# Optimization experiments

Hardware: AMD Instinct MI355X
Metric: run time of the kernel (lower is better)

Reference implementation:

```python
import jax, jax.numpy as jnp
import numpy as np

LEN = 8388608  # 2**23, must be a power of 2


def setup_inputs() -> dict:
    key = jax.random.key(0)
    k1, k2 = jax.random.split(key)
    inp = jax.random.normal(k1, (LEN,), dtype=jnp.float32)
    weight = jax.random.uniform(k2, (LEN // 2, 2), dtype=jnp.float32)  # learned twiddle factors
    return {"input": inp, "weight": weight}


def _complex_mul(a, w):
    # a: [d, cols, 2] complex pairs; w: [cols, 2] broadcast over leading dim
    ar, ai = a[:, :, 0], a[:, :, 1]
    wr, wi = w[:, 0], w[:, 1]
    return jnp.stack([ar * wr - ai * wi, ar * wi + ai * wr], axis=-1)


def reference(input, weight):
    n = input.shape[0]
    # real signal -> complex pairs, shape [n, 1, 2]
    x = jnp.stack([input, jnp.zeros_like(input)], axis=-1)[:, None, :]
    d = n // 2
    while d != 0:  # log2(n) static stages
        w = weight[0::d]          # [cols, 2] where cols == x.shape[1]
        top = x[:d]               # [d, cols, 2]
        bot = x[d:]               # [d, cols, 2]
        p = _complex_mul(bot, w)  # butterfly twiddle multiply
        x = jnp.concatenate([top + p, top - p], axis=1)  # [d, 2*cols, 2]
        d //= 2
    return x  # [1, n, 2]
```

## Files before the change

### kernel.cpp

```cpp
#include <hip/hip_runtime.h>
#include <hip/hip_fp16.h>

__device__ __forceinline__ float2 cadd(float2 a, float2 b) { return make_float2(a.x + b.x, a.y + b.y); }
__device__ __forceinline__ float2 csub(float2 a, float2 b) { return make_float2(a.x - b.x, a.y - b.y); }
__device__ __forceinline__ float2 cmul(float2 w, float2 z) {
    return make_float2(w.x * z.x - w.y * z.y, w.x * z.y + w.y * z.x);
}
__device__ __forceinline__ unsigned pk(float2 z) {
    __half2 h = __floats2half2_rn(z.x, z.y);
    return *reinterpret_cast<unsigned*>(&h);
}
__device__ __forceinline__ float2 upk(unsigned u) {
    __half2 h = *reinterpret_cast<__half2*>(&u);
    return __half22float2(h);
}


__global__ __launch_bounds__(256) void fft_pass_a(const float* __restrict__ in,
                                                  const float2* __restrict__ wt,
                                                  uint4* __restrict__ outp)
{
    __shared__ float2 L[4096];
    const int tid = threadIdx.x;
    const int l0  = blockIdx.x << 4;
    const int c   = tid & 15;
    const int qb  = tid >> 4;

    float2 pw1[4], pw2a[4], pw2b[4];
#pragma unroll
    for (int k = 0; k < 4; ++k) { pw1[k] = wt[0]; pw2a[k] = wt[0]; pw2b[k] = wt[1 << 21]; }

    {
        const int c4 = tid & 3, gg = tid >> 2;
#pragma unroll
        for (int k = 0; k < 4; ++k) {
            const int g = gg + (k << 6);
            const float4 v = *reinterpret_cast<const float4*>(in + ((size_t)g << 15) + l0 + (c4 << 2));
            const int base = (g << 4) + (c4 << 2);
            L[base + 0] = make_float2(v.x, 0.f);
            L[base + 1] = make_float2(v.y, 0.f);
            L[base + 2] = make_float2(v.z, 0.f);
            L[base + 3] = make_float2(v.w, 0.f);
        }
    }
    __syncthreads();

#pragma unroll
    for (int rho = 0; rho < 4; ++rho) {
        const int s = rho << 1, H = 128 >> s, Q = H >> 1, lo = 6 - s;
        float2 nw1[4], nw2a[4], nw2b[4];
        if (rho < 3) {
            const int s2 = s + 2, lo2 = 6 - s2;
#pragma unroll
            for (int k = 0; k < 4; ++k) {
                const int qi = (qb << 2) + k;
                const int b  = ((qi >> lo2) << (lo2 + 2)) | (qi & ((1 << lo2) - 1));
                const int jl = (int)(__brev((unsigned)(b >> (8 - s2))) >> (32 - s2));
                const int e  = jl << (21 - s2);
                nw1[k] = wt[e << 1]; nw2a[k] = wt[e]; nw2b[k] = wt[e + (1 << 21)];
            }
        }
#pragma unroll
        for (int k = 0; k < 4; ++k) {
            const int qi = (qb << 2) + k;
            const int b  = ((qi >> lo) << (lo + 2)) | (qi & ((1 << lo) - 1));
            const int iA = (b << 4) + c;
            const float2 A  = L[iA];
            const float2 Bv = L[iA + (Q << 4)];
            const float2 Cv = L[iA + (H << 4)];
            const float2 Dv = L[iA + ((H + Q) << 4)];
            const float2 pC = cmul(pw1[k], Cv), pD = cmul(pw1[k], Dv);
            const float2 tA = cadd(A, pC),  tC = csub(A, pC);
            const float2 tB = cadd(Bv, pD), tD = csub(Bv, pD);
            const float2 p2 = cmul(pw2a[k], tB);
            const float2 p3 = cmul(pw2b[k], tD);
            L[iA]                  = cadd(tA, p2);
            L[iA + (Q << 4)]       = csub(tA, p2);
            L[iA + (H << 4)]       = cadd(tC, p3);
            L[iA + ((H + Q) << 4)] = csub(tC, p3);
        }
        __syncthreads();
        if (rho < 3) {
#pragma unroll
            for (int k = 0; k < 4; ++k) { pw1[k] = nw1[k]; pw2a[k] = nw2a[k]; pw2b[k] = nw2b[k]; }
        }
    }

    {
        const int c4 = tid & 3, gg = tid >> 2;
#pragma unroll
        for (int k = 0; k < 4; ++k) {
            const int g  = gg + (k << 6);
            const int li = (g << 4) + (c4 << 2);
            uint4 v;
            v.x = pk(L[li]); v.y = pk(L[li + 1]); v.z = pk(L[li + 2]); v.w = pk(L[li + 3]);
            outp[((size_t)g << 13) + (l0 >> 2) + c4] = v;
        }
    }
}

__global__ __launch_bounds__(256) void fft_pass_b(const uint4* __restrict__ inp,
                                                  const float2* __restrict__ wt,
                                                  uint4* __restrict__ outp)
{
    __shared__ float2 L[4096];
    const int tid  = threadIdx.x;
    const int h    = blockIdx.x >> 3;
    const int l0   = (blockIdx.x & 7) << 4;
    const int hrev = (int)(__brev((unsigned)h) >> 24);
    const int c  = tid & 15;
    const int qb = tid >> 4;
    const size_t pbase = ((size_t)h << 13) + (l0 >> 2);

    float2 pw1[4], pw2a[4], pw2b[4];
    {
        const int e0 = hrev << 13;
#pragma unroll
        for (int k = 0; k < 4; ++k) { pw1[k] = wt[e0 << 1]; pw2a[k] = wt[e0]; pw2b[k] = wt[e0 + (1 << 21)]; }
    }

    {
        const int c4 = tid & 3, gg = tid >> 2;
#pragma unroll
        for (int k = 0; k < 4; ++k) {
            const int g = gg + (k << 6);
            const uint4 v = inp[pbase + (g << 5) + c4];
            const int li = (g << 4) + (c4 << 2);
            L[li]     = upk(v.x);
            L[li + 1] = upk(v.y);
            L[li + 2] = upk(v.z);
            L[li + 3] = upk(v.w);
        }
    }
    __syncthreads();

#pragma unroll
    for (int rho = 0; rho < 4; ++rho) {
        const int s = rho << 1, H = 128 >> s, Q = H >> 1, lo = 6 - s;
        float2 nw1[4], nw2a[4], nw2b[4];
        if (rho < 3) {
            const int s2 = s + 2, lo2 = 6 - s2;
#pragma unroll
            for (int k = 0; k < 4; ++k) {
                const int qi = (qb << 2) + k;
                const int b  = ((qi >> lo2) << (lo2 + 2)) | (qi & ((1 << lo2) - 1));
                const int jl = (int)(__brev((unsigned)(b >> (8 - s2))) >> (32 - s2));
                const int e  = (hrev << (13 - s2)) + (jl << (21 - s2));
                nw1[k] = wt[e << 1]; nw2a[k] = wt[e]; nw2b[k] = wt[e + (1 << 21)];
            }
        }
#pragma unroll
        for (int k = 0; k < 4; ++k) {
            const int qi = (qb << 2) + k;
            const int b  = ((qi >> lo) << (lo + 2)) | (qi & ((1 << lo) - 1));
            const int iA = (b << 4) + c;
            const float2 A  = L[iA];
            const float2 Bv = L[iA + (Q << 4)];
            const float2 Cv = L[iA + (H << 4)];
            const float2 Dv = L[iA + ((H + Q) << 4)];
            const float2 pC = cmul(pw1[k], Cv), pD = cmul(pw1[k], Dv);
            const float2 tA = cadd(A, pC),  tC = csub(A, pC);
            const float2 tB = cadd(Bv, pD), tD = csub(Bv, pD);
            const float2 p2 = cmul(pw2a[k], tB);
            const float2 p3 = cmul(pw2b[k], tD);
            L[iA]                  = cadd(tA, p2);
            L[iA + (Q << 4)]       = csub(tA, p2);
            L[iA + (H << 4)]       = cadd(tC, p3);
            L[iA + ((H + Q) << 4)] = csub(tC, p3);
        }
        __syncthreads();
        if (rho < 3) {
#pragma unroll
            for (int k = 0; k < 4; ++k) { pw1[k] = nw1[k]; pw2a[k] = nw2a[k]; pw2b[k] = nw2b[k]; }
        }
    }

    {
        const int c4 = tid & 3, gg = tid >> 2;
#pragma unroll
        for (int k = 0; k < 4; ++k) {
            const int g  = gg + (k << 6);
            const int li = (g << 4) + (c4 << 2);
            uint4 v;
            v.x = pk(L[li]); v.y = pk(L[li + 1]); v.z = pk(L[li + 2]); v.w = pk(L[li + 3]);
            outp[pbase + (g << 5) + c4] = v;
        }
    }
}

__global__ __launch_bounds__(256, 8) void fft_pass_c(const uint4* __restrict__ inp,
                                                     const float2* __restrict__ wt,
                                                     float2* __restrict__ out)
{
    __shared__ float2 L[16 * 129];
    const int tid = threadIdx.x;
    const int h0  = blockIdx.x;

    const int lam = tid & 15;
    const int bq  = tid >> 4;
    const int rH  = (h0 << 4) + lam;

    float2 pw1[2], pw2a[2], pw2b[2];
#pragma unroll
    for (int k = 0; k < 2; ++k) {
        pw1[k]  = wt[rH << 6];
        pw2a[k] = wt[rH << 5];
        pw2b[k] = wt[(rH << 5) + (1 << 21)];
    }

    {
        const int f  = tid & 31;
        const int ll = tid >> 5;
#pragma unroll
        for (int k = 0; k < 2; ++k) {
            const int lm = ll + (k << 3);
            const int H  = (int)(__brev((unsigned)((h0 << 4) + lm)) >> 16);
            const uint4 v = inp[((size_t)H << 5) + f];
            const int li = lm * 129 + (f << 2);
            L[li]     = upk(v.x);
            L[li + 1] = upk(v.y);
            L[li + 2] = upk(v.z);
            L[li + 3] = upk(v.w);
        }
    }
    __syncthreads();

    float2 pr2[4];
#pragma unroll
    for (int rho = 0; rho < 3; ++rho) {
        const int s = rho << 1, H = 64 >> s, Q = H >> 1, lo = 5 - s;
        float2 nw1[2], nw2a[2], nw2b[2];
        if (rho < 2) {
            const int s2 = s + 2, lo2 = 5 - s2;
#pragma unroll
            for (int k = 0; k < 2; ++k) {
                const int qi = (bq << 1) + k;
                const int b  = ((qi >> lo2) << (lo2 + 2)) | (qi & ((1 << lo2) - 1));
                const int jl = (int)(__brev((unsigned)(b >> (7 - s2))) >> (32 - s2));
                const int e  = (rH << (5 - s2)) + (jl << (21 - s2));
                nw1[k] = wt[e << 1]; nw2a[k] = wt[e]; nw2b[k] = wt[e + (1 << 21)];
            }
        } else {
#pragma unroll
            for (int k = 0; k < 4; ++k) {
                const int pb = (bq << 2) + k;
                const int jl = (int)(__brev((unsigned)pb) >> 26);
                pr2[k] = wt[rH + (jl << 16)];
            }
        }
#pragma unroll
        for (int k = 0; k < 2; ++k) {
            const int qi = (bq << 1) + k;
            const int b  = ((qi >> lo) << (lo + 2)) | (qi & ((1 << lo) - 1));
            const int iA = lam * 129 + b;
            const float2 A  = L[iA];
            const float2 Bv = L[iA + Q];
            const float2 Cv = L[iA + H];
            const float2 Dv = L[iA + H + Q];
            const float2 pC = cmul(pw1[k], Cv), pD = cmul(pw1[k], Dv);
            const float2 tA = cadd(A, pC),  tC = csub(A, pC);
            const float2 tB = cadd(Bv, pD), tD = csub(Bv, pD);
            const float2 p2 = cmul(pw2a[k], tB);
            const float2 p3 = cmul(pw2b[k], tD);
            L[iA]         = cadd(tA, p2);
            L[iA + Q]     = csub(tA, p2);
            L[iA + H]     = cadd(tC, p3);
            L[iA + H + Q] = csub(tC, p3);
        }
        __syncthreads();
        if (rho < 2) {
#pragma unroll
            for (int k = 0; k < 2; ++k) { pw1[k] = nw1[k]; pw2a[k] = nw2a[k]; pw2b[k] = nw2b[k]; }
        }
    }

    {
#pragma unroll
        for (int k = 0; k < 4; ++k) {
            const int pb = (bq << 2) + k;
            const int b  = pb << 1;
            const int iA = lam * 129 + b;
            const float2 A  = L[iA];
            const float2 Bv = L[iA + 1];
            const float2 p  = cmul(pr2[k], Bv);
            L[iA]     = cadd(A, p);
            L[iA + 1] = csub(A, p);
        }
    }
    __syncthreads();

    {
        const int l2 = (tid & 7) << 1;
        const int gb = tid >> 3;
#pragma unroll
        for (int k = 0; k < 4; ++k) {
            const int g    = gb + (k << 5);
            const int grev = (int)(__brev((unsigned)g) >> 25);
            const float2 a0 = L[l2 * 129 + g];
            const float2 a1 = L[(l2 + 1) * 129 + g];
            const size_t o = ((size_t)grev << 16) + (h0 << 4) + l2;
            *reinterpret_cast<float4*>(out + o) = make_float4(a0.x, a0.y, a1.x, a1.y);
        }
    }
}

extern "C" void kernel_launch(void* const* d_in, const int* in_sizes, int n_in,
                              void* d_out, int out_size, void* d_ws, size_t ws_size,
                              hipStream_t stream)
{
    (void)in_sizes; (void)n_in; (void)out_size; (void)ws_size;
    const float*  in = (const float*)d_in[0];
    const float2* wt = (const float2*)d_in[1];
    float2* outc = (float2*)d_out;
    uint4*  buf1 = (uint4*)d_ws;
    uint4*  buf2 = (uint4*)((char*)d_ws + (32u << 20));

    fft_pass_a<<<2048, 256, 0, stream>>>(in,   wt, buf1);
    fft_pass_b<<<2048, 256, 0, stream>>>(buf1, wt, buf2);
    fft_pass_c<<<4096, 256, 0, stream>>>(buf2, wt, outc);
}
```

Measured before the change: 182.4 us.

## Fuse FFT passes B and C into one register-resident 15-stage kernel

Replaces the second and third FFT passes with a single kernel in which each 1024-thread block processes a 32K-point sub-FFT. The work is split into three 5-stage radix-2 groups held in registers, separated by skewed shared-memory transposes. This removes one global-memory round trip through the fp16 intermediate buffer and one kernel launch. The cost is heavy register use (96 complex values per thread), only 256 blocks, 128KB of dynamic shared memory per block, and uncoalesced-looking strided final output writes.

```diff
diff --git a/kernel.cpp b/kernel.cpp
--- a/kernel.cpp
+++ b/kernel.cpp
@@ -13,6 +13,12 @@
 __device__ __forceinline__ float2 upk(unsigned u) {
     __half2 h = *reinterpret_cast<__half2*>(&u);
     return __half22float2(h);
+}
+
+__host__ __device__ constexpr unsigned crev(unsigned x, int bits) {
+    unsigned r = 0;
+    for (int k = 0; k < bits; ++k) r |= ((x >> k) & 1u) << (bits - 1 - k);
+    return r;
 }
 
 
@@ -99,208 +105,122 @@
     }
 }
 
-__global__ __launch_bounds__(256) void fft_pass_b(const uint4* __restrict__ inp,
-                                                  const float2* __restrict__ wt,
-                                                  uint4* __restrict__ outp)
+__global__ __launch_bounds__(1024) void fft_pass_bc(const unsigned* __restrict__ inp,
+                                                    const float2* __restrict__ wt,
+                                                    float2* __restrict__ out)
 {
-    __shared__ float2 L[4096];
-    const int tid  = threadIdx.x;
-    const int h    = blockIdx.x >> 3;
-    const int l0   = (blockIdx.x & 7) << 4;
-    const int hrev = (int)(__brev((unsigned)h) >> 24);
-    const int c  = tid & 15;
-    const int qb = tid >> 4;
-    const size_t pbase = ((size_t)h << 13) + (l0 >> 2);
-
-    float2 pw1[4], pw2a[4], pw2b[4];
-    {
-        const int e0 = hrev << 13;
-#pragma unroll
-        for (int k = 0; k < 4; ++k) { pw1[k] = wt[e0 << 1]; pw2a[k] = wt[e0]; pw2b[k] = wt[e0 + (1 << 21)]; }
-    }
-
-    {
-        const int c4 = tid & 3, gg = tid >> 2;
-#pragma unroll
-        for (int k = 0; k < 4; ++k) {
-            const int g = gg + (k << 6);
-            const uint4 v = inp[pbase + (g << 5) + c4];
-            const int li = (g << 4) + (c4 << 2);
-            L[li]     = upk(v.x);
-            L[li + 1] = upk(v.y);
-            L[li + 2] = upk(v.z);
-            L[li + 3] = upk(v.w);
-        }
-    }
-    __syncthreads();
-
-#pragma unroll
-    for (int rho = 0; rho < 4; ++rho) {
-        const int s = rho << 1, H = 128 >> s, Q = H >> 1, lo = 6 - s;
-        float2 nw1[4], nw2a[4], nw2b[4];
-        if (rho < 3) {
-            const int s2 = s + 2, lo2 = 6 - s2;
-#pragma unroll
-            for (int k = 0; k < 4; ++k) {
-                const int qi = (qb << 2) + k;
-                const int b  = ((qi >> lo2) << (lo2 + 2)) | (qi & ((1 << lo2) - 1));
-                const int jl = (int)(__brev((unsigned)(b >> (8 - s2))) >> (32 - s2));
-                const int e  = (hrev << (13 - s2)) + (jl << (21 - s2));
-                nw1[k] = wt[e << 1]; nw2a[k] = wt[e]; nw2b[k] = wt[e + (1 << 21)];
-            }
-        }
-#pragma unroll
-        for (int k = 0; k < 4; ++k) {
-            const int qi = (qb << 2) + k;
-            const int b  = ((qi >> lo) << (lo + 2)) | (qi & ((1 << lo) - 1));
-            const int iA = (b << 4) + c;
-            const float2 A  = L[iA];
-            const float2 Bv = L[iA + (Q << 4)];
-            const float2 Cv = L[iA + (H << 4)];
-            const float2 Dv = L[iA + ((H + Q) << 4)];
-            const float2 pC = cmul(pw1[k], Cv), pD = cmul(pw1[k], Dv);
-            const float2 tA = cadd(A, pC),  tC = csub(A, pC);
-            const float2 tB = cadd(Bv, pD), tD = csub(Bv, pD);
-            const float2 p2 = cmul(pw2a[k], tB);
-            const float2 p3 = cmul(pw2b[k], tD);
-            L[iA]                  = cadd(tA, p2);
-            L[iA + (Q << 4)]       = csub(tA, p2);
-            L[iA + (H << 4)]       = cadd(tC, p3);
-            L[iA + ((H + Q) << 4)] = csub(tC, p3);
-        }
-        __syncthreads();
-        if (rho < 3) {
-#pragma unroll
-            for (int k = 0; k < 4; ++k) { pw1[k] = nw1[k]; pw2a[k] = nw2a[k]; pw2b[k] = nw2b[k]; }
-        }
-    }
-
-    {
-        const int c4 = tid & 3, gg = tid >> 2;
-#pragma unroll
-        for (int k = 0; k < 4; ++k) {
-            const int g  = gg + (k << 6);
-            const int li = (g << 4) + (c4 << 2);
-            uint4 v;
-            v.x = pk(L[li]); v.y = pk(L[li + 1]); v.z = pk(L[li + 2]); v.w = pk(L[li + 3]);
-            outp[pbase + (g << 5) + c4] = v;
-        }
-    }
-}
-
-__global__ __launch_bounds__(256, 8) void fft_pass_c(const uint4* __restrict__ inp,
-                                                     const float2* __restrict__ wt,
-                                                     float2* __restrict__ out)
-{
-    __shared__ float2 L[16 * 129];
+    extern __shared__ float2 T[];
     const int tid = threadIdx.x;
-    const int h0  = blockIdx.x;
-
-    const int lam = tid & 15;
-    const int bq  = tid >> 4;
-    const int rH  = (h0 << 4) + lam;
-
-    float2 pw1[2], pw2a[2], pw2b[2];
-#pragma unroll
-    for (int k = 0; k < 2; ++k) {
-        pw1[k]  = wt[rH << 6];
-        pw2a[k] = wt[rH << 5];
-        pw2b[k] = wt[(rH << 5) + (1 << 21)];
-    }
-
-    {
-        const int f  = tid & 31;
-        const int ll = tid >> 5;
-#pragma unroll
-        for (int k = 0; k < 2; ++k) {
-            const int lm = ll + (k << 3);
-            const int H  = (int)(__brev((unsigned)((h0 << 4) + lm)) >> 16);
-            const uint4 v = inp[((size_t)H << 5) + f];
-            const int li = lm * 129 + (f << 2);
-            L[li]     = upk(v.x);
-            L[li + 1] = upk(v.y);
-            L[li + 2] = upk(v.z);
-            L[li + 3] = upk(v.w);
-        }
-    }
-    __syncthreads();
-
-    float2 pr2[4];
-#pragma unroll
-    for (int rho = 0; rho < 3; ++rho) {
-        const int s = rho << 1, H = 64 >> s, Q = H >> 1, lo = 5 - s;
-        float2 nw1[2], nw2a[2], nw2b[2];
-        if (rho < 2) {
-            const int s2 = s + 2, lo2 = 5 - s2;
-#pragma unroll
-            for (int k = 0; k < 2; ++k) {
-                const int qi = (bq << 1) + k;
-                const int b  = ((qi >> lo2) << (lo2 + 2)) | (qi & ((1 << lo2) - 1));
-                const int jl = (int)(__brev((unsigned)(b >> (7 - s2))) >> (32 - s2));
-                const int e  = (rH << (5 - s2)) + (jl << (21 - s2));
-                nw1[k] = wt[e << 1]; nw2a[k] = wt[e]; nw2b[k] = wt[e + (1 << 21)];
-            }
-        } else {
-#pragma unroll
-            for (int k = 0; k < 4; ++k) {
-                const int pb = (bq << 2) + k;
-                const int jl = (int)(__brev((unsigned)pb) >> 26);
-                pr2[k] = wt[rH + (jl << 16)];
-            }
-        }
-#pragma unroll
-        for (int k = 0; k < 2; ++k) {
-            const int qi = (bq << 1) + k;
-            const int b  = ((qi >> lo) << (lo + 2)) | (qi & ((1 << lo) - 1));
-            const int iA = lam * 129 + b;
-            const float2 A  = L[iA];
-            const float2 Bv = L[iA + Q];
-            const float2 Cv = L[iA + H];
-            const float2 Dv = L[iA + H + Q];
-            const float2 pC = cmul(pw1[k], Cv), pD = cmul(pw1[k], Dv);
-            const float2 tA = cadd(A, pC),  tC = csub(A, pC);
-            const float2 tB = cadd(Bv, pD), tD = csub(Bv, pD);
-            const float2 p2 = cmul(pw2a[k], tB);
-            const float2 p3 = cmul(pw2b[k], tD);
-            L[iA]         = cadd(tA, p2);
-            L[iA + Q]     = csub(tA, p2);
-            L[iA + H]     = cadd(tC, p3);
-            L[iA + H + Q] = csub(tC, p3);
-        }
-        __syncthreads();
-        if (rho < 2) {
-#pragma unroll
-            for (int k = 0; k < 2; ++k) { pw1[k] = nw1[k]; pw2a[k] = nw2a[k]; pw2b[k] = nw2b[k]; }
-        }
-    }
-
-    {
-#pragma unroll
-        for (int k = 0; k < 4; ++k) {
-            const int pb = (bq << 2) + k;
-            const int b  = pb << 1;
-            const int iA = lam * 129 + b;
-            const float2 A  = L[iA];
-            const float2 Bv = L[iA + 1];
-            const float2 p  = cmul(pr2[k], Bv);
-            L[iA]     = cadd(A, p);
-            L[iA + 1] = csub(A, p);
-        }
-    }
-    __syncthreads();
-
-    {
-        const int l2 = (tid & 7) << 1;
-        const int gb = tid >> 3;
-#pragma unroll
-        for (int k = 0; k < 4; ++k) {
-            const int g    = gb + (k << 5);
-            const int grev = (int)(__brev((unsigned)g) >> 25);
-            const float2 a0 = L[l2 * 129 + g];
-            const float2 a1 = L[(l2 + 1) * 129 + g];
-            const size_t o = ((size_t)grev << 16) + (h0 << 4) + l2;
-            *reinterpret_cast<float4*>(out + o) = make_float4(a0.x, a0.y, a1.x, a1.y);
-        }
+    const int h   = blockIdx.x;
+    const unsigned hrev = __brev((unsigned)h) >> 24;
+
+    float2 X[32];
+    {
+        const unsigned base = ((unsigned)h << 15) + (unsigned)tid;
+#pragma unroll
+        for (int b = 0; b < 32; ++b) X[b] = upk(inp[base + ((unsigned)b << 10)]);
+    }
+
+#pragma unroll
+    for (int s1 = 0; s1 < 5; ++s1) {
+        const int beta = 4 - s1, half = 1 << beta;
+#pragma unroll
+        for (int m = 0; m < 16; ++m) {
+            const int lo = ((m >> beta) << (beta + 1)) | (m & (half - 1));
+            const int hi = lo | half;
+            const unsigned cr = crev((unsigned)(m >> beta), s1);
+            const float2 w = wt[((cr << 8) | hrev) << (14 - s1)];
+            const float2 p = cmul(w, X[hi]);
+            X[hi] = csub(X[lo], p);
+            X[lo] = cadd(X[lo], p);
+        }
+    }
+
+    float2 Y[32];
+#pragma unroll
+    for (int b = 0; b < 16; ++b) T[(b << 10) + tid] = X[b];
+    __syncthreads();
+    if (tid < 512) {
+        const int sl = tid >> 5, v = tid & 31;
+#pragma unroll
+        for (int u = 0; u < 32; ++u) Y[u] = T[(sl << 10) + (u << 5) + v];
+    }
+    __syncthreads();
+#pragma unroll
+    for (int b = 16; b < 32; ++b) T[((b - 16) << 10) + tid] = X[b];
+    __syncthreads();
+    if (tid >= 512) {
+        const int sl = (tid >> 5) - 16, v = tid & 31;
+#pragma unroll
+        for (int u = 0; u < 32; ++u) Y[u] = T[(sl << 10) + (u << 5) + v];
+    }
+    __syncthreads();
+
+    const int b2 = tid >> 5, v2 = tid & 31;
+    const unsigned brev5b = __brev((unsigned)b2) >> 27;
+#pragma unroll
+    for (int s2 = 0; s2 < 5; ++s2) {
+        const int mu = 4 - s2, half = 1 << mu;
+#pragma unroll
+        for (int m = 0; m < 16; ++m) {
+            const int lo = ((m >> mu) << (mu + 1)) | (m & (half - 1));
+            const int hi = lo | half;
+            const unsigned cr = crev((unsigned)(m >> mu), s2);
+            const float2 w = wt[(((cr << 13) | (brev5b << 8) | hrev) << (9 - s2))];
+            const float2 p = cmul(w, Y[hi]);
+            Y[hi] = csub(Y[lo], p);
+            Y[lo] = cadd(Y[lo], p);
+        }
+    }
+
+    float2 Z[32];
+    if (b2 < 16) {
+#pragma unroll
+        for (int u = 0; u < 32; ++u)
+            T[(b2 << 10) + (u << 5) + ((u + v2) & 31)] = Y[u];
+    }
+    __syncthreads();
+    if (b2 < 16) {
+        const int u3 = tid & 31;
+#pragma unroll
+        for (int v = 0; v < 32; ++v)
+            Z[v] = T[(b2 << 10) + (u3 << 5) + ((u3 + v) & 31)];
+    }
+    __syncthreads();
+    if (b2 >= 16) {
+#pragma unroll
+        for (int u = 0; u < 32; ++u)
+            T[((b2 - 16) << 10) + (u << 5) + ((u + v2) & 31)] = Y[u];
+    }
+    __syncthreads();
+    if (b2 >= 16) {
+        const int u3 = tid & 31;
+#pragma unroll
+        for (int v = 0; v < 32; ++v)
+            Z[v] = T[((b2 - 16) << 10) + (u3 << 5) + ((u3 + v) & 31)];
+    }
+
+    const unsigned brev5u = __brev((unsigned)(tid & 31)) >> 27;
+#pragma unroll
+    for (int s3 = 0; s3 < 5; ++s3) {
+        const int nu = 4 - s3, half = 1 << nu;
+#pragma unroll
+        for (int m = 0; m < 16; ++m) {
+            const int lo = ((m >> nu) << (nu + 1)) | (m & (half - 1));
+            const int hi = lo | half;
+            const unsigned cr = crev((unsigned)(m >> nu), s3);
+            const float2 w = wt[(((cr << 18) | (brev5u << 13) | (brev5b << 8) | hrev) << (4 - s3))];
+            const float2 p = cmul(w, Z[hi]);
+            Z[hi] = csub(Z[lo], p);
+            Z[lo] = cadd(Z[lo], p);
+        }
+    }
+
+    {
+        const unsigned obase = (brev5u << 13) | (brev5b << 8) | hrev;
+#pragma unroll
+        for (int v = 0; v < 32; ++v)
+            out[(crev((unsigned)v, 5) << 18) | obase] = Z[v];
     }
 }
 
@@ -313,9 +233,14 @@
     const float2* wt = (const float2*)d_in[1];
     float2* outc = (float2*)d_out;
     uint4*  buf1 = (uint4*)d_ws;
-    uint4*  buf2 = (uint4*)((char*)d_ws + (32u << 20));
-
-    fft_pass_a<<<2048, 256, 0, stream>>>(in,   wt, buf1);
-    fft_pass_b<<<2048, 256, 0, stream>>>(buf1, wt, buf2);
-    fft_pass_c<<<4096, 256, 0, stream>>>(buf2, wt, outc);
-}
+
+    static bool attr_done = false;
+    if (!attr_done) {
+        (void)hipFuncSetAttribute(reinterpret_cast<const void*>(fft_pass_bc),
+                                  hipFuncAttributeMaxDynamicSharedMemorySize, 131072);
+        attr_done = true;
+    }
+
+    fft_pass_a<<<2048, 256, 0, stream>>>(in, wt, buf1);
+    fft_pass_bc<<<256, 1024, 131072, stream>>>((const unsigned*)buf1, wt, outc);
+}
```

Result: slower. 321.7 us (+76.4%).

## Split middle FFT pass into two in-place register-resident radix kernels

Applied to the files above, without the earlier changes.

Replaces the shared-memory middle pass (8 stages via LDS with syncs) with two in-place kernels: a 32-point register FFT (5 stages) and an 8-point register FFT (3 stages), both working directly on the fp16 workspace. This removes the LDS traffic and barriers and the second workspace buffer. In exchange it adds a kernel launch and one more full read/write of the 32 MB fp16 intermediate, plus strided 4-byte global accesses instead of 16-byte vector loads.

```diff
diff --git a/kernel.cpp b/kernel.cpp
--- a/kernel.cpp
+++ b/kernel.cpp
@@ -13,6 +13,12 @@
 __device__ __forceinline__ float2 upk(unsigned u) {
     __half2 h = *reinterpret_cast<__half2*>(&u);
     return __half22float2(h);
+}
+
+__host__ __device__ constexpr unsigned crev(unsigned x, int bits) {
+    unsigned r = 0;
+    for (int k = 0; k < bits; ++k) r |= ((x >> k) & 1u) << (bits - 1 - k);
+    return r;
 }
 
 
@@ -99,93 +105,82 @@
     }
 }
 
-__global__ __launch_bounds__(256) void fft_pass_b(const uint4* __restrict__ inp,
-                                                  const float2* __restrict__ wt,
-                                                  uint4* __restrict__ outp)
-{
-    __shared__ float2 L[4096];
-    const int tid  = threadIdx.x;
-    const int h    = blockIdx.x >> 3;
-    const int l0   = (blockIdx.x & 7) << 4;
-    const int hrev = (int)(__brev((unsigned)h) >> 24);
-    const int c  = tid & 15;
-    const int qb = tid >> 4;
-    const size_t pbase = ((size_t)h << 13) + (l0 >> 2);
-
-    float2 pw1[4], pw2a[4], pw2b[4];
-    {
-        const int e0 = hrev << 13;
-#pragma unroll
-        for (int k = 0; k < 4; ++k) { pw1[k] = wt[e0 << 1]; pw2a[k] = wt[e0]; pw2b[k] = wt[e0 + (1 << 21)]; }
-    }
-
-    {
-        const int c4 = tid & 3, gg = tid >> 2;
-#pragma unroll
-        for (int k = 0; k < 4; ++k) {
-            const int g = gg + (k << 6);
-            const uint4 v = inp[pbase + (g << 5) + c4];
-            const int li = (g << 4) + (c4 << 2);
-            L[li]     = upk(v.x);
-            L[li + 1] = upk(v.y);
-            L[li + 2] = upk(v.z);
-            L[li + 3] = upk(v.w);
-        }
-    }
-    __syncthreads();
-
-#pragma unroll
-    for (int rho = 0; rho < 4; ++rho) {
-        const int s = rho << 1, H = 128 >> s, Q = H >> 1, lo = 6 - s;
-        float2 nw1[4], nw2a[4], nw2b[4];
-        if (rho < 3) {
-            const int s2 = s + 2, lo2 = 6 - s2;
-#pragma unroll
-            for (int k = 0; k < 4; ++k) {
-                const int qi = (qb << 2) + k;
-                const int b  = ((qi >> lo2) << (lo2 + 2)) | (qi & ((1 << lo2) - 1));
-                const int jl = (int)(__brev((unsigned)(b >> (8 - s2))) >> (32 - s2));
-                const int e  = (hrev << (13 - s2)) + (jl << (21 - s2));
-                nw1[k] = wt[e << 1]; nw2a[k] = wt[e]; nw2b[k] = wt[e + (1 << 21)];
-            }
-        }
-#pragma unroll
-        for (int k = 0; k < 4; ++k) {
-            const int qi = (qb << 2) + k;
-            const int b  = ((qi >> lo) << (lo + 2)) | (qi & ((1 << lo) - 1));
-            const int iA = (b << 4) + c;
-            const float2 A  = L[iA];
-            const float2 Bv = L[iA + (Q << 4)];
-            const float2 Cv = L[iA + (H << 4)];
-            const float2 Dv = L[iA + ((H + Q) << 4)];
-            const float2 pC = cmul(pw1[k], Cv), pD = cmul(pw1[k], Dv);
-            const float2 tA = cadd(A, pC),  tC = csub(A, pC);
-            const float2 tB = cadd(Bv, pD), tD = csub(Bv, pD);
-            const float2 p2 = cmul(pw2a[k], tB);
-            const float2 p3 = cmul(pw2b[k], tD);
-            L[iA]                  = cadd(tA, p2);
-            L[iA + (Q << 4)]       = csub(tA, p2);
-            L[iA + (H << 4)]       = cadd(tC, p3);
-            L[iA + ((H + Q) << 4)] = csub(tC, p3);
-        }
-        __syncthreads();
-        if (rho < 3) {
-#pragma unroll
-            for (int k = 0; k < 4; ++k) { pw1[k] = nw1[k]; pw2a[k] = nw2a[k]; pw2b[k] = nw2b[k]; }
-        }
-    }
-
-    {
-        const int c4 = tid & 3, gg = tid >> 2;
-#pragma unroll
-        for (int k = 0; k < 4; ++k) {
-            const int g  = gg + (k << 6);
-            const int li = (g << 4) + (c4 << 2);
-            uint4 v;
-            v.x = pk(L[li]); v.y = pk(L[li + 1]); v.z = pk(L[li + 2]); v.w = pk(L[li + 3]);
-            outp[pbase + (g << 5) + c4] = v;
-        }
-    }
+__global__ __launch_bounds__(256) void fft_pass_b1(unsigned* __restrict__ buf,
+                                                   const float2* __restrict__ wt)
+{
+    const int tid = threadIdx.x;
+    const int h   = blockIdx.x >> 2;
+    const int low = ((blockIdx.x & 3) << 8) | tid;
+    const unsigned hrev = __brev((unsigned)h) >> 24;
+    const unsigned base = ((unsigned)h << 15) | (unsigned)low;
+
+    float2 X[32];
+#pragma unroll
+    for (int m = 0; m < 32; ++m) X[m] = upk(buf[base + ((unsigned)m << 10)]);
+
+#pragma unroll
+    for (int s = 0; s < 5; ++s) {
+        const int half = 1 << (4 - s);
+#pragma unroll
+        for (int j = 0; j < 16; ++j) {
+            const int mh = j >> (4 - s);
+            const int lo = (mh << (5 - s)) | (j & (half - 1));
+            const int hi = lo | half;
+            const unsigned cr = crev((unsigned)mh, s);
+            const float2 w = wt[(((cr << 8) | hrev) << (14 - s))];
+            const float2 p = cmul(w, X[hi]);
+            X[hi] = csub(X[lo], p);
+            X[lo] = cadd(X[lo], p);
+        }
+    }
+#pragma unroll
+    for (int m = 0; m < 32; ++m) buf[base + ((unsigned)m << 10)] = pk(X[m]);
+}
+
+__global__ __launch_bounds__(256) void fft_pass_b2(unsigned* __restrict__ buf,
+                                                   const float2* __restrict__ wt)
+{
+    const int tid = threadIdx.x;
+    const int P   = __builtin_amdgcn_readfirstlane((blockIdx.x << 1) | (tid >> 7));
+    const int r   = tid & 127;
+    const unsigned R = __brev((unsigned)P) >> 19;
+    const unsigned base = ((unsigned)P << 10) | (unsigned)r;
+
+    float2 X[8];
+#pragma unroll
+    for (int n = 0; n < 8; ++n) X[n] = upk(buf[base + ((unsigned)n << 7)]);
+
+    {
+        const float2 w = wt[R << 9];
+#pragma unroll
+        for (int n = 0; n < 4; ++n) {
+            const float2 p = cmul(w, X[n + 4]);
+            X[n + 4] = csub(X[n], p);
+            X[n]     = cadd(X[n], p);
+        }
+    }
+#pragma unroll
+    for (int n2 = 0; n2 < 2; ++n2) {
+        const float2 w = wt[(((unsigned)n2 << 13) | R) << 8];
+#pragma unroll
+        for (int u = 0; u < 2; ++u) {
+            const int lo = (n2 << 2) + u, hi = lo + 2;
+            const float2 p = cmul(w, X[hi]);
+            X[hi] = csub(X[lo], p);
+            X[lo] = cadd(X[lo], p);
+        }
+    }
+#pragma unroll
+    for (int q = 0; q < 4; ++q) {
+        const float2 w = wt[((crev((unsigned)q, 2) << 13) | R) << 7];
+        const int lo = q << 1, hi = lo + 1;
+        const float2 p = cmul(w, X[hi]);
+        X[hi] = csub(X[lo], p);
+        X[lo] = cadd(X[lo], p);
+    }
+
+#pragma unroll
+    for (int n = 0; n < 8; ++n) buf[base + ((unsigned)n << 7)] = pk(X[n]);
 }
 
 __global__ __launch_bounds__(256, 8) void fft_pass_c(const uint4* __restrict__ inp,
@@ -313,9 +308,10 @@
     const float2* wt = (const float2*)d_in[1];
     float2* outc = (float2*)d_out;
     uint4*  buf1 = (uint4*)d_ws;
-    uint4*  buf2 = (uint4*)((char*)d_ws + (32u << 20));
-
-    fft_pass_a<<<2048, 256, 0, stream>>>(in,   wt, buf1);
-    fft_pass_b<<<2048, 256, 0, stream>>>(buf1, wt, buf2);
-    fft_pass_c<<<4096, 256, 0, stream>>>(buf2, wt, outc);
-}
+    unsigned* buf1w = (unsigned*)d_ws;
+
+    fft_pass_a <<<2048, 256, 0, stream>>>(in, wt, buf1);
+    fft_pass_b1<<<1024, 256, 0, stream>>>(buf1w, wt);
+    fft_pass_b2<<<4096, 256, 0, stream>>>(buf1w, wt);
+    fft_pass_c <<<4096, 256, 0, stream>>>(buf1, wt, outc);
+}
```

Measured after the change: 203.2 us. 11.4% more time.
